# Optimization experiments

Hardware: AMD Instinct MI355X
Metric: run time of the kernel (lower is better)

The kernel has to match this reference:

```python
import math
import jax, jax.numpy as jnp
import numpy as np

N_HEADS = 16
D_EMBED = 1024
D_HEAD = D_EMBED // N_HEADS
B, S = 4, 2048


def setup_inputs() -> dict:
    key = jax.random.key(0)
    k1, k2, k3, k4, k5 = jax.random.split(key, 5)
    scale_in = 1.0 / math.sqrt(D_EMBED)
    return {
        "x": jax.random.normal(k1, (B, S, D_EMBED), dtype=jnp.float32),
        "w_in": jax.random.normal(k2, (3 * D_EMBED, D_EMBED), dtype=jnp.float32) * scale_in,
        "b_in": jax.random.normal(k3, (3 * D_EMBED,), dtype=jnp.float32) * 0.02,
        "w_out": jax.random.normal(k4, (D_EMBED, D_EMBED), dtype=jnp.float32) * scale_in,
        "b_out": jax.random.normal(k5, (D_EMBED,), dtype=jnp.float32) * 0.02,
        "causal_mask": 1,
    }


def reference(x, w_in, b_in, w_out, b_out, causal_mask):
    Bn, Sn, D = x.shape
    # fused QKV projection (torch Linear: x @ W.T + b)
    qkv = x @ w_in.T + b_in                       # (B, S, 3D)
    q, k, v = jnp.split(qkv, 3, axis=-1)
    def to_heads(t):
        return t.reshape(Bn, Sn, N_HEADS, D_HEAD).transpose(0, 2, 1, 3)  # (B,H,S,dh)
    q, k, v = to_heads(q), to_heads(k), to_heads(v)
    # manual scaled dot-product attention, full (B,H,S,S) scores
    scores = jnp.einsum("bhqd,bhkd->bhqk", q, k)
    if causal_mask:
        tri = jnp.triu(jnp.ones((Sn, Sn), dtype=bool), k=1)
        scores = jnp.where(tri, -jnp.inf, scores)
    scores = scores / math.sqrt(D_HEAD)
    weights = jax.nn.softmax(scores, axis=-1)
    out = jnp.einsum("bhqk,bhkd->bhqd", weights, v)  # (B,H,S,dh)
    out = out.transpose(0, 2, 1, 3).reshape(Bn, Sn, D)
    return out @ w_out.T + b_out
```

## Files before the change

kernel.cpp:

```cpp
#include <hip/hip_runtime.h>

typedef __bf16 bf16x8 __attribute__((ext_vector_type(8)));
typedef float  f32x4  __attribute__((ext_vector_type(4)));
typedef unsigned int uint;

__device__ inline unsigned short f2bf(float f) {
  union { float f; unsigned int u; } v; v.f = f;
  unsigned int u = v.u;
  unsigned int r = u + 0x7FFF + ((u >> 16) & 1);
  return (unsigned short)(r >> 16);
}

__device__ inline uint pack_bf16_rhu(float a, float b) {
  uint ua = __builtin_bit_cast(uint, a) + 0x8000u;
  uint ub = __builtin_bit_cast(uint, b) + 0x8000u;
  return __builtin_amdgcn_perm(ub, ua, 0x07060302u);
}

__device__ inline void load_lds16(const unsigned short* g, unsigned short* l) {
  __builtin_amdgcn_global_load_lds(
      (const __attribute__((address_space(1))) uint*)(g),
      (__attribute__((address_space(3))) uint*)(l), 16, 0, 0);
}

__device__ inline void cvt4(const float* in, unsigned short* out) {
  float4 f = *reinterpret_cast<const float4*>(in);
  ushort4 o;
  o.x = f2bf(f.x); o.y = f2bf(f.y); o.z = f2bf(f.z); o.w = f2bf(f.w);
  *reinterpret_cast<ushort4*>(out) = o;
}

__global__ void cvt_all(const float* __restrict__ x, const float* __restrict__ w_in,
                        const float* __restrict__ w_out,
                        unsigned short* __restrict__ x_bf,
                        unsigned short* __restrict__ w_in_bf,
                        unsigned short* __restrict__ w_out_bf) {
  const int n1 = 8192 * 1024, n2 = 3072 * 1024;
  int i = (blockIdx.x * blockDim.x + threadIdx.x) * 4;
  if (i < n1)            cvt4(x + i, x_bf + i);
  else if (i < n1 + n2)  cvt4(w_in + (i - n1), w_in_bf + (i - n1));
  else                   cvt4(w_out + (i - n1 - n2), w_out_bf + (i - n1 - n2));
}

template<bool OUT_BF16>
__global__ __launch_bounds__(256) void gemm_bt128(
    const unsigned short* __restrict__ A,
    const unsigned short* __restrict__ B,
    const float* __restrict__ bias,
    void* __restrict__ Cout,
    int M, int N, int K, int ldc, float scale, int ncut)
{
  __shared__ __attribute__((aligned(16))) unsigned short As[128 * 64];
  __shared__ __attribute__((aligned(16))) unsigned short Bs[128 * 64];

  const int t    = threadIdx.x;
  const int wave = t >> 6, lane = t & 63;
  const int l16  = lane & 15, quad = lane >> 4;
  const int wr = wave >> 1, wc = wave & 1;
  const int m0 = blockIdx.y * 128, n0 = blockIdx.x * 128;
  const int l8 = l16 & 7;

  f32x4 acc[4][4] = {};

  for (int k0 = 0; k0 < K; k0 += 64) {
#pragma unroll
    for (int i = 0; i < 4; ++i) {
      int chunk = i * 256 + t;
      int row = chunk >> 3, cb = chunk & 7;
      int gcb = cb ^ (row & 7);
      load_lds16(A + (size_t)(m0 + row) * K + k0 + gcb * 8, As + chunk * 8);
    }
#pragma unroll
    for (int i = 0; i < 4; ++i) {
      int chunk = i * 256 + t;
      int row = chunk >> 3, cb = chunk & 7;
      int gcb = cb ^ (row & 7);
      load_lds16(B + (size_t)(n0 + row) * K + k0 + gcb * 8, Bs + chunk * 8);
    }
    __syncthreads();
#pragma unroll
    for (int ks = 0; ks < 2; ++ks) {
      bf16x8 af[4], bfr[4];
#pragma unroll
      for (int mt = 0; mt < 4; ++mt)
        af[mt] = *(const bf16x8*)(As + (wr * 64 + mt * 16 + l16) * 64 +
                                  (((ks * 4 + quad) ^ l8) << 3));
#pragma unroll
      for (int nt = 0; nt < 4; ++nt)
        bfr[nt] = *(const bf16x8*)(Bs + (wc * 64 + nt * 16 + l16) * 64 +
                                   (((ks * 4 + quad) ^ l8) << 3));
#pragma unroll
      for (int mt = 0; mt < 4; ++mt)
#pragma unroll
        for (int nt = 0; nt < 4; ++nt)
          acc[mt][nt] = __builtin_amdgcn_mfma_f32_16x16x32_bf16(af[mt], bfr[nt], acc[mt][nt], 0, 0, 0);
    }
    __syncthreads();
  }

#pragma unroll
  for (int nt = 0; nt < 4; ++nt) {
    int col = n0 + wc * 64 + nt * 16 + l16;
    float bv = bias[col];
    float mlt = (col < ncut) ? scale : 1.0f;
#pragma unroll
    for (int mt = 0; mt < 4; ++mt) {
#pragma unroll
      for (int r = 0; r < 4; ++r) {
        int row = m0 + wr * 64 + mt * 16 + quad * 4 + r;
        float v = (acc[mt][nt][r] + bv) * mlt;
        if (OUT_BF16)
          ((unsigned short*)Cout)[(size_t)row * ldc + col] = f2bf(v);
        else
          ((float*)Cout)[(size_t)row * ldc + col] = v;
      }
    }
  }
}

__global__ __launch_bounds__(256) void vtrans(const unsigned short* __restrict__ qkv,
                                              unsigned short* __restrict__ vt) {
  __shared__ unsigned short Ls[64][72];
  const int t = threadIdx.x;
  const int s0 = blockIdx.x * 64;
  const int bh = blockIdx.y, b = bh >> 4, h = bh & 15;
  {
    int s = t >> 2, c = (t & 3) * 16;
    const unsigned short* src = qkv + ((size_t)(b * 2048 + s0 + s)) * 3072 + 2048 + h * 64 + c;
    *(uint4*)&Ls[s][c]     = *(const uint4*)src;
    *(uint4*)&Ls[s][c + 8] = *(const uint4*)(src + 8);
  }
  __syncthreads();
  {
    int d = t >> 2, sb = (t & 3) * 16;
    unsigned short tmp[16];
#pragma unroll
    for (int i = 0; i < 16; ++i) tmp[i] = Ls[sb + i][d];
    size_t base = ((size_t)bh * 64 + d) * 2048 + s0 + sb;
    *(uint4*)(vt + base)     = *(const uint4*)tmp;
    *(uint4*)(vt + base + 8) = *(const uint4*)(tmp + 8);
  }
}

__global__ __launch_bounds__(256) void attn(
    const unsigned short* __restrict__ qkv,
    const unsigned short* __restrict__ vt,
    unsigned short* __restrict__ y,
    const int* __restrict__ flag)
{
  __shared__ __attribute__((aligned(16))) unsigned short Qs[64][72];
  __shared__ __attribute__((aligned(16))) unsigned short Ks[64][72];
  __shared__ __attribute__((aligned(16))) unsigned short VtF[64 * 64];

  const int t    = threadIdx.x;
  const int wave = t >> 6, lane = t & 63;
  const int l16  = lane & 15, quad = lane >> 4;
  const int idx = blockIdx.x;
  const int bh  = idx & 63;
  const int qt  = 31 - (idx >> 6);
  const int b = bh >> 4, h = bh & 15;
  const int causal = flag[0];
  const int q0 = qt * 64;

  const unsigned short* Qg = qkv + (size_t)b * 2048 * 3072 + h * 64;
  const unsigned short* Kg = Qg + 1024;
  const unsigned short* Vtg = vt + (size_t)bh * 64 * 2048;

  {
    int r = t >> 2, c = (t & 3) * 16;
    const unsigned short* src = Qg + (size_t)(q0 + r) * 3072 + c;
    *(uint4*)&Qs[r][c]     = *(const uint4*)src;
    *(uint4*)&Qs[r][c + 8] = *(const uint4*)(src + 8);
  }
  __syncthreads();
  bf16x8 qf[2];
  qf[0] = *(const bf16x8*)&Qs[wave * 16 + l16][quad * 8];
  qf[1] = *(const bf16x8*)&Qs[wave * 16 + l16][32 + quad * 8];
  __syncthreads();
  unsigned short (*Ps)[72] = Qs;

  f32x4 ot[4] = {};
  float l_lane = 0.f;
  const int q_glob = q0 + wave * 16 + l16;
  const int jmax = causal ? qt : 31;

  const int kr = t >> 2, kc = (t & 3) * 16;
  const int vd = t >> 2, vb = t & 3;
  const int vpos0 = ((vb     + vd) & 7) << 3;
  const int vpos1 = ((vb + 4 + vd) & 7) << 3;
  const unsigned short* vrow = Vtg + (size_t)vd * 2048;

  uint4 kreg0, kreg1, vreg0, vreg1;
  {
    const unsigned short* src = Kg + (size_t)kr * 3072 + kc;
    kreg0 = *(const uint4*)src;
    kreg1 = *(const uint4*)(src + 8);
    vreg0 = *(const uint4*)(vrow + vb * 8);
    vreg1 = *(const uint4*)(vrow + vb * 8 + 32);
  }

  for (int j = 0; j <= jmax; ++j) {
    *(uint4*)&Ks[kr][kc]     = kreg0;
    *(uint4*)&Ks[kr][kc + 8] = kreg1;
    *(uint4*)(VtF + vd * 64 + vpos0) = vreg0;
    *(uint4*)(VtF + vd * 64 + vpos1) = vreg1;
    __syncthreads();

    if (j < jmax) {
      const int kvn = (j + 1) * 64;
      const unsigned short* src = Kg + (size_t)(kvn + kr) * 3072 + kc;
      kreg0 = *(const uint4*)src;
      kreg1 = *(const uint4*)(src + 8);
      vreg0 = *(const uint4*)(vrow + kvn + vb * 8);
      vreg1 = *(const uint4*)(vrow + kvn + vb * 8 + 32);
    }

    f32x4 st[4] = {};
#pragma unroll
    for (int ks = 0; ks < 2; ++ks) {
#pragma unroll
      for (int mt = 0; mt < 4; ++mt) {
        bf16x8 kf = *(const bf16x8*)&Ks[mt * 16 + l16][ks * 32 + quad * 8];
        st[mt] = __builtin_amdgcn_mfma_f32_16x16x32_bf16(kf, qf[ks], st[mt], 0, 0, 0);
      }
    }

    const bool diag = (causal != 0) && (j == qt);
    const int kv0 = j * 64;
#pragma unroll
    for (int mt = 0; mt < 4; ++mt) {
      float p[4];
#pragma unroll
      for (int r = 0; r < 4; ++r) {
        float pv = __builtin_amdgcn_exp2f(st[mt][r]);
        if (diag) {
          int kv = kv0 + mt * 16 + quad * 4 + r;
          if (kv > q_glob) pv = 0.f;
        }
        p[r] = pv;
      }
      l_lane += (p[0] + p[1]) + (p[2] + p[3]);
      uint2 w;
      w.x = pack_bf16_rhu(p[0], p[1]);
      w.y = pack_bf16_rhu(p[2], p[3]);
      *(uint2*)&Ps[wave * 16 + l16][mt * 16 + quad * 4] = w;
    }
    __threadfence_block();

#pragma unroll
    for (int ks = 0; ks < 2; ++ks) {
      bf16x8 pf = *(const bf16x8*)&Ps[wave * 16 + l16][ks * 32 + quad * 8];
#pragma unroll
      for (int mt = 0; mt < 4; ++mt) {
        int pos = ((ks * 4 + quad + l16) & 7) << 3;
        bf16x8 vf = *(const bf16x8*)(VtF + (mt * 16 + l16) * 64 + pos);
        ot[mt] = __builtin_amdgcn_mfma_f32_16x16x32_bf16(vf, pf, ot[mt], 0, 0, 0);
      }
    }
    __syncthreads();
  }

  l_lane += __shfl_xor(l_lane, 16);
  l_lane += __shfl_xor(l_lane, 32);
  float inv = 1.f / l_lane;

#pragma unroll
  for (int mt = 0; mt < 4; ++mt) {
    uint2 w;
    w.x = pack_bf16_rhu(ot[mt][0] * inv, ot[mt][1] * inv);
    w.y = pack_bf16_rhu(ot[mt][2] * inv, ot[mt][3] * inv);
    *(uint2*)&Ps[wave * 16 + l16][mt * 16 + quad * 4] = w;
  }
  __syncthreads();
  {
    int r = t >> 2, c = (t & 3) * 16;
    size_t base = ((size_t)b * 2048 + q0 + r) * 1024 + h * 64 + c;
    *(uint4*)(y + base)     = *(const uint4*)&Ps[r][c];
    *(uint4*)(y + base + 8) = *(const uint4*)&Ps[r][c + 8];
  }
}

extern "C" void kernel_launch(void* const* d_in, const int* in_sizes, int n_in,
                              void* d_out, int out_size, void* d_ws, size_t ws_size,
                              hipStream_t stream) {
  const float* x     = (const float*)d_in[0];
  const float* w_in  = (const float*)d_in[1];
  const float* b_in  = (const float*)d_in[2];
  const float* w_out = (const float*)d_in[3];
  const float* b_out = (const float*)d_in[4];
  const int*   cmask = (const int*)d_in[5];

  char* ws = (char*)d_ws;
  unsigned short* x_bf     = (unsigned short*)(ws);
  unsigned short* w_in_bf  = (unsigned short*)(ws + 16777216);
  unsigned short* w_out_bf = (unsigned short*)(ws + 23068672);
  unsigned short* qkv_bf   = (unsigned short*)(ws + 25165824);
  unsigned short* y_bf     = (unsigned short*)(ws + 75497472);
  unsigned short* vt_bf    = x_bf;

  const int ntot = (8192 + 3072 + 1024) * 1024;
  cvt_all<<<dim3(ntot / 4 / 256), 256, 0, stream>>>(x, w_in, w_out, x_bf, w_in_bf, w_out_bf);

  gemm_bt128<true><<<dim3(24, 64), 256, 0, stream>>>(
      x_bf, w_in_bf, b_in, qkv_bf, 8192, 3072, 1024, 3072,
      0.18033688011112042f, 1024);

  vtrans<<<dim3(32, 64), 256, 0, stream>>>(qkv_bf, vt_bf);

  attn<<<dim3(2048), 256, 0, stream>>>(qkv_bf, vt_bf, y_bf, cmask);

  gemm_bt128<false><<<dim3(8, 64), 256, 0, stream>>>(
      y_bf, w_out_bf, b_out, d_out, 8192, 1024, 1024, 1024, 1.0f, 0);
}
```

Measured before the change: 262.2 us.

## Fuse V transpose into QKV GEMM epilogue and process 128 query rows per block

The QKV projection epilogue now writes the V slice directly in transposed per-head layout, with Q/K stored in a narrower 2048-wide buffer, so the separate vtrans kernel and its extra read/write of V go away. The attention kernel now handles 128 query rows per block (two 16-row subtiles per wave). This reuses each K/V tile load across twice as many queries and halves the grid. Tiles are scheduled in a custom interleaved order to balance causal work. The costs are more registers and LDS per block, fewer blocks to spread across CUs, and scattered 8-byte stores for V in the GEMM epilogue.

```diff
diff --git a/kernel.cpp b/kernel.cpp
--- a/kernel.cpp
+++ b/kernel.cpp
@@ -42,12 +42,13 @@
   else                   cvt4(w_out + (i - n1 - n2), w_out_bf + (i - n1 - n2));
 }
 
-template<bool OUT_BF16>
+template<bool OUT_BF16, bool VSPLIT>
 __global__ __launch_bounds__(256) void gemm_bt128(
     const unsigned short* __restrict__ A,
     const unsigned short* __restrict__ B,
     const float* __restrict__ bias,
     void* __restrict__ Cout,
+    unsigned short* __restrict__ vt,
     int M, int N, int K, int ldc, float scale, int ncut)
 {
   __shared__ __attribute__((aligned(16))) unsigned short As[128 * 64];
@@ -105,50 +106,39 @@
     float mlt = (col < ncut) ? scale : 1.0f;
 #pragma unroll
     for (int mt = 0; mt < 4; ++mt) {
-#pragma unroll
-      for (int r = 0; r < 4; ++r) {
-        int row = m0 + wr * 64 + mt * 16 + quad * 4 + r;
-        float v = (acc[mt][nt][r] + bv) * mlt;
-        if (OUT_BF16)
-          ((unsigned short*)Cout)[(size_t)row * ldc + col] = f2bf(v);
-        else
-          ((float*)Cout)[(size_t)row * ldc + col] = v;
+      int row0 = m0 + wr * 64 + mt * 16 + quad * 4;
+      float v0 = (acc[mt][nt][0] + bv) * mlt;
+      float v1 = (acc[mt][nt][1] + bv) * mlt;
+      float v2 = (acc[mt][nt][2] + bv) * mlt;
+      float v3 = (acc[mt][nt][3] + bv) * mlt;
+      if (VSPLIT && col >= 2048) {
+        int d = col - 2048, h = d >> 6, dd = d & 63;
+        int bb = row0 >> 11, s = row0 & 2047;
+        uint2 w;
+        w.x = pack_bf16_rhu(v0, v1);
+        w.y = pack_bf16_rhu(v2, v3);
+        *(uint2*)(vt + ((size_t)((bb * 16 + h) * 64 + dd) * 2048 + s)) = w;
+      } else {
+#pragma unroll
+        for (int r = 0; r < 4; ++r) {
+          float v = (r == 0) ? v0 : (r == 1) ? v1 : (r == 2) ? v2 : v3;
+          if (OUT_BF16)
+            ((unsigned short*)Cout)[(size_t)(row0 + r) * ldc + col] = f2bf(v);
+          else
+            ((float*)Cout)[(size_t)(row0 + r) * ldc + col] = v;
+        }
       }
     }
   }
 }
 
-__global__ __launch_bounds__(256) void vtrans(const unsigned short* __restrict__ qkv,
-                                              unsigned short* __restrict__ vt) {
-  __shared__ unsigned short Ls[64][72];
-  const int t = threadIdx.x;
-  const int s0 = blockIdx.x * 64;
-  const int bh = blockIdx.y, b = bh >> 4, h = bh & 15;
-  {
-    int s = t >> 2, c = (t & 3) * 16;
-    const unsigned short* src = qkv + ((size_t)(b * 2048 + s0 + s)) * 3072 + 2048 + h * 64 + c;
-    *(uint4*)&Ls[s][c]     = *(const uint4*)src;
-    *(uint4*)&Ls[s][c + 8] = *(const uint4*)(src + 8);
-  }
-  __syncthreads();
-  {
-    int d = t >> 2, sb = (t & 3) * 16;
-    unsigned short tmp[16];
-#pragma unroll
-    for (int i = 0; i < 16; ++i) tmp[i] = Ls[sb + i][d];
-    size_t base = ((size_t)bh * 64 + d) * 2048 + s0 + sb;
-    *(uint4*)(vt + base)     = *(const uint4*)tmp;
-    *(uint4*)(vt + base + 8) = *(const uint4*)(tmp + 8);
-  }
-}
-
 __global__ __launch_bounds__(256) void attn(
-    const unsigned short* __restrict__ qkv,
+    const unsigned short* __restrict__ qkv2,
     const unsigned short* __restrict__ vt,
     unsigned short* __restrict__ y,
     const int* __restrict__ flag)
 {
-  __shared__ __attribute__((aligned(16))) unsigned short Qs[64][72];
+  __shared__ __attribute__((aligned(16))) unsigned short Qs[128][72];
   __shared__ __attribute__((aligned(16))) unsigned short Ks[64][72];
   __shared__ __attribute__((aligned(16))) unsigned short VtF[64 * 64];
 
@@ -157,32 +147,37 @@
   const int l16  = lane & 15, quad = lane >> 4;
   const int idx = blockIdx.x;
   const int bh  = idx & 63;
-  const int qt  = 31 - (idx >> 6);
+  const int g   = idx >> 6, ph = g >> 2, gr = g & 3;
+  const int qt  = (ph == 0) ? (15 - gr) : (ph == 1) ? gr : (ph == 2) ? (11 - gr) : (4 + gr);
   const int b = bh >> 4, h = bh & 15;
   const int causal = flag[0];
-  const int q0 = qt * 64;
-
-  const unsigned short* Qg = qkv + (size_t)b * 2048 * 3072 + h * 64;
+  const int q0 = qt * 128;
+
+  const unsigned short* Qg = qkv2 + (size_t)b * 2048 * 2048 + h * 64;
   const unsigned short* Kg = Qg + 1024;
   const unsigned short* Vtg = vt + (size_t)bh * 64 * 2048;
 
   {
-    int r = t >> 2, c = (t & 3) * 16;
-    const unsigned short* src = Qg + (size_t)(q0 + r) * 3072 + c;
-    *(uint4*)&Qs[r][c]     = *(const uint4*)src;
-    *(uint4*)&Qs[r][c + 8] = *(const uint4*)(src + 8);
+    int r = t >> 1, c0 = (t & 1) * 32;
+    const unsigned short* src = Qg + (size_t)(q0 + r) * 2048 + c0;
+#pragma unroll
+    for (int i = 0; i < 4; ++i)
+      *(uint4*)&Qs[r][c0 + i * 8] = *(const uint4*)(src + i * 8);
   }
   __syncthreads();
-  bf16x8 qf[2];
-  qf[0] = *(const bf16x8*)&Qs[wave * 16 + l16][quad * 8];
-  qf[1] = *(const bf16x8*)&Qs[wave * 16 + l16][32 + quad * 8];
+  bf16x8 qf[2][2];
+#pragma unroll
+  for (int su = 0; su < 2; ++su) {
+    qf[su][0] = *(const bf16x8*)&Qs[wave * 32 + su * 16 + l16][quad * 8];
+    qf[su][1] = *(const bf16x8*)&Qs[wave * 32 + su * 16 + l16][32 + quad * 8];
+  }
   __syncthreads();
   unsigned short (*Ps)[72] = Qs;
 
-  f32x4 ot[4] = {};
-  float l_lane = 0.f;
-  const int q_glob = q0 + wave * 16 + l16;
-  const int jmax = causal ? qt : 31;
+  f32x4 ot[2][4] = {};
+  float l_lane[2] = {0.f, 0.f};
+  const int qg0 = q0 + wave * 32 + l16;
+  const int jmax = causal ? (2 * qt + 1) : 31;
 
   const int kr = t >> 2, kc = (t & 3) * 16;
   const int vd = t >> 2, vb = t & 3;
@@ -192,7 +187,7 @@
 
   uint4 kreg0, kreg1, vreg0, vreg1;
   {
-    const unsigned short* src = Kg + (size_t)kr * 3072 + kc;
+    const unsigned short* src = Kg + (size_t)kr * 2048 + kc;
     kreg0 = *(const uint4*)src;
     kreg1 = *(const uint4*)(src + 8);
     vreg0 = *(const uint4*)(vrow + vb * 8);
@@ -208,75 +203,86 @@
 
     if (j < jmax) {
       const int kvn = (j + 1) * 64;
-      const unsigned short* src = Kg + (size_t)(kvn + kr) * 3072 + kc;
+      const unsigned short* src = Kg + (size_t)(kvn + kr) * 2048 + kc;
       kreg0 = *(const uint4*)src;
       kreg1 = *(const uint4*)(src + 8);
       vreg0 = *(const uint4*)(vrow + kvn + vb * 8);
       vreg1 = *(const uint4*)(vrow + kvn + vb * 8 + 32);
     }
 
-    f32x4 st[4] = {};
+    f32x4 st[2][4] = {};
 #pragma unroll
     for (int ks = 0; ks < 2; ++ks) {
 #pragma unroll
       for (int mt = 0; mt < 4; ++mt) {
         bf16x8 kf = *(const bf16x8*)&Ks[mt * 16 + l16][ks * 32 + quad * 8];
-        st[mt] = __builtin_amdgcn_mfma_f32_16x16x32_bf16(kf, qf[ks], st[mt], 0, 0, 0);
+        st[0][mt] = __builtin_amdgcn_mfma_f32_16x16x32_bf16(kf, qf[0][ks], st[0][mt], 0, 0, 0);
+        st[1][mt] = __builtin_amdgcn_mfma_f32_16x16x32_bf16(kf, qf[1][ks], st[1][mt], 0, 0, 0);
       }
     }
 
-    const bool diag = (causal != 0) && (j == qt);
+    const bool diag = (causal != 0) && (j >= 2 * qt);
     const int kv0 = j * 64;
 #pragma unroll
-    for (int mt = 0; mt < 4; ++mt) {
-      float p[4];
-#pragma unroll
-      for (int r = 0; r < 4; ++r) {
-        float pv = __builtin_amdgcn_exp2f(st[mt][r]);
-        if (diag) {
-          int kv = kv0 + mt * 16 + quad * 4 + r;
-          if (kv > q_glob) pv = 0.f;
+    for (int su = 0; su < 2; ++su) {
+      const int qg = qg0 + su * 16;
+#pragma unroll
+      for (int mt = 0; mt < 4; ++mt) {
+        float p[4];
+#pragma unroll
+        for (int r = 0; r < 4; ++r) {
+          float pv = __builtin_amdgcn_exp2f(st[su][mt][r]);
+          if (diag) {
+            int kv = kv0 + mt * 16 + quad * 4 + r;
+            if (kv > qg) pv = 0.f;
+          }
+          p[r] = pv;
         }
-        p[r] = pv;
+        l_lane[su] += (p[0] + p[1]) + (p[2] + p[3]);
+        uint2 w;
+        w.x = pack_bf16_rhu(p[0], p[1]);
+        w.y = pack_bf16_rhu(p[2], p[3]);
+        *(uint2*)&Ps[wave * 32 + su * 16 + l16][mt * 16 + quad * 4] = w;
       }
-      l_lane += (p[0] + p[1]) + (p[2] + p[3]);
-      uint2 w;
-      w.x = pack_bf16_rhu(p[0], p[1]);
-      w.y = pack_bf16_rhu(p[2], p[3]);
-      *(uint2*)&Ps[wave * 16 + l16][mt * 16 + quad * 4] = w;
     }
     __threadfence_block();
 
 #pragma unroll
     for (int ks = 0; ks < 2; ++ks) {
-      bf16x8 pf = *(const bf16x8*)&Ps[wave * 16 + l16][ks * 32 + quad * 8];
+      bf16x8 pf0 = *(const bf16x8*)&Ps[wave * 32 + l16][ks * 32 + quad * 8];
+      bf16x8 pf1 = *(const bf16x8*)&Ps[wave * 32 + 16 + l16][ks * 32 + quad * 8];
 #pragma unroll
       for (int mt = 0; mt < 4; ++mt) {
         int pos = ((ks * 4 + quad + l16) & 7) << 3;
         bf16x8 vf = *(const bf16x8*)(VtF + (mt * 16 + l16) * 64 + pos);
-        ot[mt] = __builtin_amdgcn_mfma_f32_16x16x32_bf16(vf, pf, ot[mt], 0, 0, 0);
+        ot[0][mt] = __builtin_amdgcn_mfma_f32_16x16x32_bf16(vf, pf0, ot[0][mt], 0, 0, 0);
+        ot[1][mt] = __builtin_amdgcn_mfma_f32_16x16x32_bf16(vf, pf1, ot[1][mt], 0, 0, 0);
       }
     }
     __syncthreads();
   }
 
-  l_lane += __shfl_xor(l_lane, 16);
-  l_lane += __shfl_xor(l_lane, 32);
-  float inv = 1.f / l_lane;
-
-#pragma unroll
-  for (int mt = 0; mt < 4; ++mt) {
-    uint2 w;
-    w.x = pack_bf16_rhu(ot[mt][0] * inv, ot[mt][1] * inv);
-    w.y = pack_bf16_rhu(ot[mt][2] * inv, ot[mt][3] * inv);
-    *(uint2*)&Ps[wave * 16 + l16][mt * 16 + quad * 4] = w;
+#pragma unroll
+  for (int su = 0; su < 2; ++su) {
+    float l = l_lane[su];
+    l += __shfl_xor(l, 16);
+    l += __shfl_xor(l, 32);
+    float inv = 1.f / l;
+#pragma unroll
+    for (int mt = 0; mt < 4; ++mt) {
+      uint2 w;
+      w.x = pack_bf16_rhu(ot[su][mt][0] * inv, ot[su][mt][1] * inv);
+      w.y = pack_bf16_rhu(ot[su][mt][2] * inv, ot[su][mt][3] * inv);
+      *(uint2*)&Ps[wave * 32 + su * 16 + l16][mt * 16 + quad * 4] = w;
+    }
   }
   __syncthreads();
   {
-    int r = t >> 2, c = (t & 3) * 16;
-    size_t base = ((size_t)b * 2048 + q0 + r) * 1024 + h * 64 + c;
-    *(uint4*)(y + base)     = *(const uint4*)&Ps[r][c];
-    *(uint4*)(y + base + 8) = *(const uint4*)&Ps[r][c + 8];
+    int r = t >> 1, c0 = (t & 1) * 32;
+    size_t base = ((size_t)b * 2048 + q0 + r) * 1024 + h * 64 + c0;
+#pragma unroll
+    for (int i = 0; i < 4; ++i)
+      *(uint4*)(y + base + i * 8) = *(const uint4*)&Ps[r][c0 + i * 8];
   }
 }
 
@@ -294,21 +300,19 @@
   unsigned short* x_bf     = (unsigned short*)(ws);
   unsigned short* w_in_bf  = (unsigned short*)(ws + 16777216);
   unsigned short* w_out_bf = (unsigned short*)(ws + 23068672);
-  unsigned short* qkv_bf   = (unsigned short*)(ws + 25165824);
+  unsigned short* qkv2_bf  = (unsigned short*)(ws + 25165824);
+  unsigned short* vt_bf    = (unsigned short*)(ws + 58720256);
   unsigned short* y_bf     = (unsigned short*)(ws + 75497472);
-  unsigned short* vt_bf    = x_bf;
 
   const int ntot = (8192 + 3072 + 1024) * 1024;
   cvt_all<<<dim3(ntot / 4 / 256), 256, 0, stream>>>(x, w_in, w_out, x_bf, w_in_bf, w_out_bf);
 
-  gemm_bt128<true><<<dim3(24, 64), 256, 0, stream>>>(
-      x_bf, w_in_bf, b_in, qkv_bf, 8192, 3072, 1024, 3072,
+  gemm_bt128<true, true><<<dim3(24, 64), 256, 0, stream>>>(
+      x_bf, w_in_bf, b_in, qkv2_bf, vt_bf, 8192, 3072, 1024, 2048,
       0.18033688011112042f, 1024);
 
-  vtrans<<<dim3(32, 64), 256, 0, stream>>>(qkv_bf, vt_bf);
-
-  attn<<<dim3(2048), 256, 0, stream>>>(qkv_bf, vt_bf, y_bf, cmask);
-
-  gemm_bt128<false><<<dim3(8, 64), 256, 0, stream>>>(
-      y_bf, w_out_bf, b_out, d_out, 8192, 1024, 1024, 1024, 1.0f, 0);
-}
+  attn<<<dim3(1024), 256, 0, stream>>>(qkv2_bf, vt_bf, y_bf, cmask);
+
+  gemm_bt128<false, false><<<dim3(8, 64), 256, 0, stream>>>(
+      y_bf, w_out_bf, b_out, d_out, nullptr, 8192, 1024, 1024, 1024, 1.0f, 0);
+}
```

New measurement: 259.9 us. No clear change (-0.9%).
